# Kernel tuning notes

Hardware: AMD Instinct MI355X
Metric: run time of the kernel (lower is better)

Reference implementation:

```python
import jax, jax.numpy as jnp
import numpy as np


def _cdist_p2(x, y):
    # x: [B, N, D], y: [B, M, D] -> [B, N, M] euclidean distances
    x2 = jnp.sum(x * x, axis=-1, keepdims=True)          # [B, N, 1]
    y2 = jnp.sum(y * y, axis=-1, keepdims=True)          # [B, M, 1]
    xy = jnp.einsum('bnd,bmd->bnm', x, y)                # [B, N, M]
    d2 = x2 + jnp.swapaxes(y2, -1, -2) - 2.0 * xy
    return jnp.sqrt(jnp.maximum(d2, 0.0))


def setup_inputs() -> dict:
    key = jax.random.key(0)
    kx, ky = jax.random.split(key)
    B, N, M, D = 8, 8192, 8192, 64
    x = jax.random.normal(kx, (B, N, D), dtype=jnp.float32)
    y = jax.random.normal(ky, (B, M, D), dtype=jnp.float32)
    return {"x": x, "y": y}


def reference(x, y):
    # relative_distances: [B, N, M]
    rd = _cdist_p2(x, y)
    M = rd.shape[-1]
    a = jnp.min(rd, axis=-1)            # [B, N] nearest y for each x
    b = jnp.min(rd, axis=-2)            # [B, M] nearest x for each y
    loss_per_batch = jnp.sum(a, axis=-1) + jnp.sum(b, axis=-1)  # [B]
    return jnp.mean(loss_per_batch) / M
```

## Files before the change

### kernel.cpp

```cpp
#include <hip/hip_runtime.h>
#include <cstdint>
#include <cstddef>

typedef unsigned short u16;
typedef __attribute__((ext_vector_type(8))) short short8;
typedef __attribute__((ext_vector_type(8))) u16 ushort8;
typedef __attribute__((ext_vector_type(4))) float float4_t;

#define BB 8
#define NN 8192
#define DD 64
#define NTILES 64
#define TILE_SHORTS 8192

__device__ inline u16 f32_to_bf16(float f) {
  unsigned u = __float_as_uint(f);
  u += 0x7FFFu + ((u >> 16) & 1u);
  return (u16)(u >> 16);
}

__device__ inline unsigned enc_ord(float f) {
  unsigned u = __float_as_uint(f);
  return (u & 0x80000000u) ? ~u : (u | 0x80000000u);
}
__device__ inline float dec_ord(unsigned u) {
  return __uint_as_float((u & 0x80000000u) ? (u & 0x7fffffffu) : ~u);
}

__global__ void zero_kernel(unsigned* __restrict__ p, int n) {
  int i = blockIdx.x * 256 + threadIdx.x;
  if (i < n) p[i] = 0u;
}

__global__ __launch_bounds__(256) void pre_kernel(
    const float* __restrict__ x, const float* __restrict__ y,
    u16* __restrict__ xs, u16* __restrict__ ys,
    float* __restrict__ x2h, float* __restrict__ y2h)
{
  const int bid = blockIdx.x;
  const int tid = threadIdx.x;
  const bool isY = bid >= 256;
  const float* src = isY ? y : x;
  u16* dst = isY ? ys : xs;
  float* s2 = isY ? y2h : x2h;

  const int row = ((bid & 255) << 8) | tid;
  const float4* rp = (const float4*)(src + (size_t)row * DD);
  float buf[DD];
  float ss = 0.f;
#pragma unroll
  for (int k = 0; k < 16; ++k) {
    float4 f = rp[k];
    buf[4*k+0] = f.x; buf[4*k+1] = f.y; buf[4*k+2] = f.z; buf[4*k+3] = f.w;
    ss += f.x*f.x + f.y*f.y + f.z*f.z + f.w*f.w;
  }
  s2[row] = 0.5f * ss;

  const int b  = row >> 13;
  const int n  = row & (NN - 1);
  const int nt = n >> 7;
  const int I  = (n >> 4) & 7;
  const int rl = n & 15;
  u16* tb = dst + (size_t)((b << 6) | nt) * TILE_SHORTS;
#pragma unroll
  for (int s = 0; s < 2; ++s)
#pragma unroll
    for (int qq = 0; qq < 4; ++qq) {
      ushort8 o;
#pragma unroll
      for (int j = 0; j < 8; ++j) o[j] = f32_to_bf16(buf[s*32 + qq*8 + j]);
      *(ushort8*)(tb + (I*2 + s)*512 + (qq*16 + rl)*8) = o;
    }
}

__global__ __launch_bounds__(256, 2) void main_kernel(
    const u16* __restrict__ xs, const u16* __restrict__ ys,
    const float* __restrict__ x2h, const float* __restrict__ y2h,
    float* __restrict__ a_min, float* __restrict__ colpart,
    unsigned* __restrict__ colmax_u, const int use_part)
{
  __shared__ __align__(16) u16 ytile[2][TILE_SHORTS];
  __shared__ float colbuf[2][2][128];
  __shared__ float rowbuf[2][128];

  const int bid = blockIdx.x;
  const int b   = bid & 7;
  const int nt  = bid >> 3;
  const int tid = threadIdx.x;
  const int w = tid >> 6, lane = tid & 63;
  const int wr = w >> 1, wc = w & 1;
  const int l15 = lane & 15, q = lane >> 4;
  const int n0 = nt << 7;

  const u16* xs_tile = xs + (size_t)((b << 6) | nt) * TILE_SHORTS;
  short8 afr[4][2];
#pragma unroll
  for (int i = 0; i < 4; ++i)
#pragma unroll
    for (int s = 0; s < 2; ++s)
      afr[i][s] = *(const short8*)(xs_tile + ((wr*4 + i)*2 + s)*512 + lane*8);

  float x2r[4][4];
  const float* x2b = x2h + b*NN + n0 + wr*64;
#pragma unroll
  for (int i = 0; i < 4; ++i)
#pragma unroll
    for (int r = 0; r < 4; ++r) x2r[i][r] = x2b[i*16 + q*4 + r];

  float rowmax[4][4];
#pragma unroll
  for (int i = 0; i < 4; ++i)
#pragma unroll
    for (int r = 0; r < 4; ++r) rowmax[i][r] = -3.0e38f;

  const float* y2b = y2h + b*NN;
  const u16* ys_b  = ys + (size_t)(b << 6) * TILE_SHORTS;

#pragma unroll
  for (int c = 0; c < 4; ++c) {
    const int chunk = w*4 + c;
    __builtin_amdgcn_global_load_lds(
        (const __attribute__((address_space(1))) void*)(ys_b + chunk*512 + lane*8),
        (__attribute__((address_space(3))) void*)(&ytile[0][chunk*512]),
        16, 0, 0);
  }
  __syncthreads();

  const float4_t zero4 = {0.f, 0.f, 0.f, 0.f};
  int cur = 0;
  for (int mt = 0; mt < NTILES; ++mt) {
    if (mt + 1 < NTILES) {
      const u16* g = ys_b + (size_t)(mt + 1) * TILE_SHORTS;
#pragma unroll
      for (int c = 0; c < 4; ++c) {
        const int chunk = w*4 + c;
        __builtin_amdgcn_global_load_lds(
            (const __attribute__((address_space(1))) void*)(g + chunk*512 + lane*8),
            (__attribute__((address_space(3))) void*)(&ytile[cur ^ 1][chunk*512]),
            16, 0, 0);
      }
    }

    float y2c[4];
#pragma unroll
    for (int j = 0; j < 4; ++j) y2c[j] = y2b[(mt << 7) + wc*64 + j*16 + l15];

    short8 bf[4][2];
#pragma unroll
    for (int j = 0; j < 4; ++j)
#pragma unroll
      for (int s = 0; s < 2; ++s)
        bf[j][s] = *(const short8*)(&ytile[cur][((wc*4 + j)*2 + s)*512 + lane*8]);

    float4_t acc[4][4];
#pragma unroll
    for (int i = 0; i < 4; ++i)
#pragma unroll
      for (int j = 0; j < 4; ++j)
        acc[i][j] = __builtin_amdgcn_mfma_f32_16x16x32_bf16(afr[i][0], bf[j][0], zero4, 0, 0, 0);
#pragma unroll
    for (int i = 0; i < 4; ++i)
#pragma unroll
      for (int j = 0; j < 4; ++j)
        acc[i][j] = __builtin_amdgcn_mfma_f32_16x16x32_bf16(afr[i][1], bf[j][1], acc[i][j], 0, 0, 0);

    float cmax[4] = {-3.0e38f, -3.0e38f, -3.0e38f, -3.0e38f};
#pragma unroll
    for (int i = 0; i < 4; ++i)
#pragma unroll
      for (int j = 0; j < 4; ++j)
#pragma unroll
        for (int r = 0; r < 4; ++r) {
          float v = acc[i][j][r];
          rowmax[i][r] = fmaxf(rowmax[i][r], v - y2c[j]);
          cmax[j]      = fmaxf(cmax[j],      v - x2r[i][r]);
        }
#pragma unroll
    for (int j = 0; j < 4; ++j) {
      cmax[j] = fmaxf(cmax[j], __shfl_xor(cmax[j], 16));
      cmax[j] = fmaxf(cmax[j], __shfl_xor(cmax[j], 32));
    }
    float lo = (q & 1) ? cmax[1] : cmax[0];
    float hi = (q & 1) ? cmax[3] : cmax[2];
    float cv = (q & 2) ? hi : lo;
    colbuf[mt & 1][wr][wc*64 + lane] = cv;
    __syncthreads();
    if (tid < 128) {
      float v = fmaxf(colbuf[mt & 1][0][tid], colbuf[mt & 1][1][tid]);
      const int m = (mt << 7) + tid;
      if (use_part) colpart[(size_t)((b << 6) | nt) * NN + m] = v;
      else          atomicMax(&colmax_u[b*NN + m], enc_ord(v));
    }
    cur ^= 1;
  }

#pragma unroll
  for (int i = 0; i < 4; ++i)
#pragma unroll
    for (int r = 0; r < 4; ++r) {
      float v = rowmax[i][r];
      v = fmaxf(v, __shfl_xor(v, 1));
      v = fmaxf(v, __shfl_xor(v, 2));
      v = fmaxf(v, __shfl_xor(v, 4));
      v = fmaxf(v, __shfl_xor(v, 8));
      rowmax[i][r] = v;
    }
  if (l15 == 0) {
#pragma unroll
    for (int i = 0; i < 4; ++i)
#pragma unroll
      for (int r = 0; r < 4; ++r)
        rowbuf[wc][wr*64 + i*16 + q*4 + r] = rowmax[i][r];
  }
  __syncthreads();
  if (tid < 128) {
    float v  = fmaxf(rowbuf[0][tid], rowbuf[1][tid]);
    float x2 = x2h[b*NN + n0 + tid];
    a_min[b*NN + n0 + tid] = sqrtf(fmaxf(2.f*(x2 - v), 0.f));
  }
}

__global__ __launch_bounds__(256) void reduce_kernel(
    const float* __restrict__ colpart, const unsigned* __restrict__ colmax_u,
    const float* __restrict__ y2h, const float* __restrict__ a_min,
    float* __restrict__ partials, const int use_part)
{
  const int bid = blockIdx.x;
  const int tid = threadIdx.x;
  const int b = bid >> 5, mc = bid & 31;
  const int m = (mc << 8) + tid;

  float v;
  if (use_part) {
    v = -3.0e38f;
#pragma unroll 4
    for (int nt = 0; nt < 64; ++nt)
      v = fmaxf(v, colpart[(size_t)((b << 6) | nt) * NN + m]);
  } else {
    v = dec_ord(colmax_u[b*NN + m]);
  }
  float s = sqrtf(fmaxf(2.f*(y2h[b*NN + m] - v), 0.f));
  s += a_min[bid*256 + tid];

#pragma unroll
  for (int d = 1; d < 64; d <<= 1) s += __shfl_xor(s, d);
  __shared__ float wsum[4];
  if ((tid & 63) == 0) wsum[tid >> 6] = s;
  __syncthreads();
  if (tid == 0) partials[bid] = wsum[0] + wsum[1] + wsum[2] + wsum[3];
}

__global__ void final_kernel(const float* __restrict__ partials, float* __restrict__ out) {
  const int tid = threadIdx.x;
  float s = partials[tid];
#pragma unroll
  for (int d = 1; d < 64; d <<= 1) s += __shfl_xor(s, d);
  __shared__ float wsum[4];
  if ((tid & 63) == 0) wsum[tid >> 6] = s;
  __syncthreads();
  if (tid == 0) out[0] = (wsum[0] + wsum[1] + wsum[2] + wsum[3]) * (1.0f / 65536.0f);
}

extern "C" void kernel_launch(void* const* d_in, const int* in_sizes, int n_in,
                              void* d_out, int out_size, void* d_ws, size_t ws_size,
                              hipStream_t stream) {
  const float* x = (const float*)d_in[0];
  const float* y = (const float*)d_in[1];
  float* out = (float*)d_out;

  char* p = (char*)d_ws;
  u16* xs = (u16*)p;            p += (size_t)512 * 16384;
  u16* ys = (u16*)p;            p += (size_t)512 * 16384;
  float* x2h = (float*)p;       p += (size_t)65536 * 4;
  float* y2h = (float*)p;       p += (size_t)65536 * 4;
  float* a_min = (float*)p;     p += (size_t)65536 * 4;
  float* partials = (float*)p;  p += 4096;
  unsigned* colmax_u = (unsigned*)p;
  float* colpart = (float*)p;
  const size_t base = (size_t)(p - (char*)d_ws);
  const int use_part = (ws_size >= base + (size_t)16777216) ? 1 : 0;

  if (!use_part)
    zero_kernel<<<dim3(256), dim3(256), 0, stream>>>(colmax_u, 65536);

  pre_kernel<<<dim3(512), dim3(256), 0, stream>>>(x, y, xs, ys, x2h, y2h);
  main_kernel<<<dim3(512), dim3(256), 0, stream>>>(xs, ys, x2h, y2h, a_min,
                                                   colpart, colmax_u, use_part);
  reduce_kernel<<<dim3(256), dim3(256), 0, stream>>>(colpart, colmax_u, y2h,
                                                     a_min, partials, use_part);
  final_kernel<<<dim3(1), dim3(256), 0, stream>>>(partials, out);
}
```

Baseline: 193.7 us.

## Split main kernel over three M ranges and fold x2 bias into MFMA

The main kernel's M loop is split into three ranges, which triples the grid to 1536 blocks and raises occupancy to 3 blocks per CU. Row-min partials are combined later in the reduce kernel, through partial buffers or atomics. The -x2 term is fed as the MFMA accumulator init, so the column max needs no per-element subtraction. The y2 values are now staged into LDS together with the tile. pre_kernel is also spread over four threads per row to raise parallelism. In exchange the kernel writes more partial data, and the extra occupancy may bring register pressure.

```diff
diff --git a/kernel.cpp b/kernel.cpp
--- a/kernel.cpp
+++ b/kernel.cpp
@@ -12,6 +12,7 @@
 #define DD 64
 #define NTILES 64
 #define TILE_SHORTS 8192
+#define TILE_EXT 8448
 
 __device__ inline u16 f32_to_bf16(float f) {
   unsigned u = __float_as_uint(f);
@@ -39,53 +40,62 @@
 {
   const int bid = blockIdx.x;
   const int tid = threadIdx.x;
-  const bool isY = bid >= 256;
+  const bool isY = bid >= 1024;
   const float* src = isY ? y : x;
   u16* dst = isY ? ys : xs;
   float* s2 = isY ? y2h : x2h;
 
-  const int row = ((bid & 255) << 8) | tid;
-  const float4* rp = (const float4*)(src + (size_t)row * DD);
-  float buf[DD];
+  const int row = ((bid & 1023) << 6) | (tid >> 2);
+  const int kq  = tid & 3;
+
+  const float4* rp = (const float4*)(src + (size_t)row * DD + kq * 16);
+  float buf[16];
   float ss = 0.f;
 #pragma unroll
-  for (int k = 0; k < 16; ++k) {
+  for (int k = 0; k < 4; ++k) {
     float4 f = rp[k];
     buf[4*k+0] = f.x; buf[4*k+1] = f.y; buf[4*k+2] = f.z; buf[4*k+3] = f.w;
     ss += f.x*f.x + f.y*f.y + f.z*f.z + f.w*f.w;
   }
-  s2[row] = 0.5f * ss;
+  ss += __shfl_xor(ss, 1);
+  ss += __shfl_xor(ss, 2);
+  if (kq == 0) s2[row] = 0.5f * ss;
 
   const int b  = row >> 13;
   const int n  = row & (NN - 1);
   const int nt = n >> 7;
   const int I  = (n >> 4) & 7;
   const int rl = n & 15;
+  const int s  = kq >> 1;
+  const int qq0 = (kq & 1) * 2;
   u16* tb = dst + (size_t)((b << 6) | nt) * TILE_SHORTS;
 #pragma unroll
-  for (int s = 0; s < 2; ++s)
-#pragma unroll
-    for (int qq = 0; qq < 4; ++qq) {
-      ushort8 o;
-#pragma unroll
-      for (int j = 0; j < 8; ++j) o[j] = f32_to_bf16(buf[s*32 + qq*8 + j]);
-      *(ushort8*)(tb + (I*2 + s)*512 + (qq*16 + rl)*8) = o;
-    }
-}
-
-__global__ __launch_bounds__(256, 2) void main_kernel(
+  for (int t = 0; t < 2; ++t) {
+    ushort8 o;
+#pragma unroll
+    for (int j = 0; j < 8; ++j) o[j] = f32_to_bf16(buf[t*8 + j]);
+    *(ushort8*)(tb + (I*2 + s)*512 + ((qq0 + t)*16 + rl)*8) = o;
+  }
+}
+
+__global__ __launch_bounds__(256, 3) void main_kernel(
     const u16* __restrict__ xs, const u16* __restrict__ ys,
     const float* __restrict__ x2h, const float* __restrict__ y2h,
-    float* __restrict__ a_min, float* __restrict__ colpart,
-    unsigned* __restrict__ colmax_u, const int use_part)
+    float* __restrict__ rowpart, float* __restrict__ colpart,
+    unsigned* __restrict__ rowmax_u, unsigned* __restrict__ colmax_u,
+    const int use_part)
 {
-  __shared__ __align__(16) u16 ytile[2][TILE_SHORTS];
+  __shared__ __align__(16) u16 ytile[2][TILE_EXT];
   __shared__ float colbuf[2][2][128];
   __shared__ float rowbuf[2][128];
 
   const int bid = blockIdx.x;
   const int b   = bid & 7;
-  const int nt  = bid >> 3;
+  const int nt  = (bid >> 3) & 63;
+  const int h   = bid >> 9;
+  const int mt_start = (h == 0) ? 0 : (h == 1 ? 22 : 43);
+  const int mt_end   = (h == 0) ? 22 : (h == 1 ? 43 : 64);
+
   const int tid = threadIdx.x;
   const int w = tid >> 6, lane = tid & 63;
   const int wr = w >> 1, wc = w & 1;
@@ -100,12 +110,13 @@
     for (int s = 0; s < 2; ++s)
       afr[i][s] = *(const short8*)(xs_tile + ((wr*4 + i)*2 + s)*512 + lane*8);
 
-  float x2r[4][4];
+  float4_t negx2[4];
   const float* x2b = x2h + b*NN + n0 + wr*64;
 #pragma unroll
-  for (int i = 0; i < 4; ++i)
-#pragma unroll
-    for (int r = 0; r < 4; ++r) x2r[i][r] = x2b[i*16 + q*4 + r];
+  for (int i = 0; i < 4; ++i) {
+    float4_t v = *(const float4_t*)(x2b + i*16 + q*4);
+    negx2[i] = {-v[0], -v[1], -v[2], -v[3]};
+  }
 
   float rowmax[4][4];
 #pragma unroll
@@ -116,20 +127,27 @@
   const float* y2b = y2h + b*NN;
   const u16* ys_b  = ys + (size_t)(b << 6) * TILE_SHORTS;
 
-#pragma unroll
-  for (int c = 0; c < 4; ++c) {
-    const int chunk = w*4 + c;
-    __builtin_amdgcn_global_load_lds(
-        (const __attribute__((address_space(1))) void*)(ys_b + chunk*512 + lane*8),
-        (__attribute__((address_space(3))) void*)(&ytile[0][chunk*512]),
-        16, 0, 0);
+  {
+    const u16* g = ys_b + (size_t)mt_start * TILE_SHORTS;
+#pragma unroll
+    for (int c = 0; c < 4; ++c) {
+      const int chunk = w*4 + c;
+      __builtin_amdgcn_global_load_lds(
+          (const __attribute__((address_space(1))) void*)(g + chunk*512 + lane*8),
+          (__attribute__((address_space(3))) void*)(&ytile[0][chunk*512]),
+          16, 0, 0);
+    }
+    if (w == 0 && lane < 32)
+      __builtin_amdgcn_global_load_lds(
+          (const __attribute__((address_space(1))) void*)(y2b + mt_start*128 + lane*4),
+          (__attribute__((address_space(3))) void*)(&ytile[0][TILE_SHORTS]),
+          16, 0, 0);
   }
   __syncthreads();
 
-  const float4_t zero4 = {0.f, 0.f, 0.f, 0.f};
   int cur = 0;
-  for (int mt = 0; mt < NTILES; ++mt) {
-    if (mt + 1 < NTILES) {
+  for (int mt = mt_start; mt < mt_end; ++mt) {
+    if (mt + 1 < mt_end) {
       const u16* g = ys_b + (size_t)(mt + 1) * TILE_SHORTS;
 #pragma unroll
       for (int c = 0; c < 4; ++c) {
@@ -139,11 +157,17 @@
             (__attribute__((address_space(3))) void*)(&ytile[cur ^ 1][chunk*512]),
             16, 0, 0);
       }
-    }
-
+      if (w == 0 && lane < 32)
+        __builtin_amdgcn_global_load_lds(
+            (const __attribute__((address_space(1))) void*)(y2b + (mt+1)*128 + lane*4),
+            (__attribute__((address_space(3))) void*)(&ytile[cur ^ 1][TILE_SHORTS]),
+            16, 0, 0);
+    }
+
+    const float* y2t = (const float*)&ytile[cur][TILE_SHORTS];
     float y2c[4];
 #pragma unroll
-    for (int j = 0; j < 4; ++j) y2c[j] = y2b[(mt << 7) + wc*64 + j*16 + l15];
+    for (int j = 0; j < 4; ++j) y2c[j] = y2t[wc*64 + j*16 + l15];
 
     short8 bf[4][2];
 #pragma unroll
@@ -157,24 +181,33 @@
     for (int i = 0; i < 4; ++i)
 #pragma unroll
       for (int j = 0; j < 4; ++j)
-        acc[i][j] = __builtin_amdgcn_mfma_f32_16x16x32_bf16(afr[i][0], bf[j][0], zero4, 0, 0, 0);
+        acc[i][j] = __builtin_amdgcn_mfma_f32_16x16x32_bf16(afr[i][0], bf[j][0], negx2[i], 0, 0, 0);
 #pragma unroll
     for (int i = 0; i < 4; ++i)
 #pragma unroll
       for (int j = 0; j < 4; ++j)
         acc[i][j] = __builtin_amdgcn_mfma_f32_16x16x32_bf16(afr[i][1], bf[j][1], acc[i][j], 0, 0, 0);
 
-    float cmax[4] = {-3.0e38f, -3.0e38f, -3.0e38f, -3.0e38f};
+    float cmax[4];
+#pragma unroll
+    for (int j = 0; j < 4; ++j) {
+      float m0 = fmaxf(fmaxf(acc[0][j][0], acc[0][j][1]), fmaxf(acc[0][j][2], acc[0][j][3]));
+      float m1 = fmaxf(fmaxf(acc[1][j][0], acc[1][j][1]), fmaxf(acc[1][j][2], acc[1][j][3]));
+      float m2 = fmaxf(fmaxf(acc[2][j][0], acc[2][j][1]), fmaxf(acc[2][j][2], acc[2][j][3]));
+      float m3 = fmaxf(fmaxf(acc[3][j][0], acc[3][j][1]), fmaxf(acc[3][j][2], acc[3][j][3]));
+      cmax[j] = fmaxf(fmaxf(m0, m1), fmaxf(m2, m3));
+    }
 #pragma unroll
     for (int i = 0; i < 4; ++i)
 #pragma unroll
-      for (int j = 0; j < 4; ++j)
-#pragma unroll
-        for (int r = 0; r < 4; ++r) {
-          float v = acc[i][j][r];
-          rowmax[i][r] = fmaxf(rowmax[i][r], v - y2c[j]);
-          cmax[j]      = fmaxf(cmax[j],      v - x2r[i][r]);
-        }
+      for (int r = 0; r < 4; ++r) {
+        float t0 = acc[i][0][r] - y2c[0];
+        float t1 = acc[i][1][r] - y2c[1];
+        float t2 = acc[i][2][r] - y2c[2];
+        float t3 = acc[i][3][r] - y2c[3];
+        rowmax[i][r] = fmaxf(fmaxf(rowmax[i][r], fmaxf(t0, t1)), fmaxf(t2, t3));
+      }
+
 #pragma unroll
     for (int j = 0; j < 4; ++j) {
       cmax[j] = fmaxf(cmax[j], __shfl_xor(cmax[j], 16));
@@ -214,33 +247,40 @@
   }
   __syncthreads();
   if (tid < 128) {
-    float v  = fmaxf(rowbuf[0][tid], rowbuf[1][tid]);
-    float x2 = x2h[b*NN + n0 + tid];
-    a_min[b*NN + n0 + tid] = sqrtf(fmaxf(2.f*(x2 - v), 0.f));
+    float v = fmaxf(rowbuf[0][tid], rowbuf[1][tid]);
+    if (use_part) rowpart[(size_t)(h*512 + (b << 6) + nt) * 128 + tid] = v;
+    else          atomicMax(&rowmax_u[b*NN + n0 + tid], enc_ord(v));
   }
 }
 
 __global__ __launch_bounds__(256) void reduce_kernel(
-    const float* __restrict__ colpart, const unsigned* __restrict__ colmax_u,
-    const float* __restrict__ y2h, const float* __restrict__ a_min,
+    const float* __restrict__ rowpart, const float* __restrict__ colpart,
+    const unsigned* __restrict__ rowmax_u, const unsigned* __restrict__ colmax_u,
+    const float* __restrict__ y2h,
     float* __restrict__ partials, const int use_part)
 {
   const int bid = blockIdx.x;
   const int tid = threadIdx.x;
-  const int b = bid >> 5, mc = bid & 31;
-  const int m = (mc << 8) + tid;
-
-  float v;
+  const int g = bid*256 + tid;
+  const int b = g >> 13, m = g & (NN - 1);
+
+  float vc, vr;
   if (use_part) {
-    v = -3.0e38f;
-#pragma unroll 4
+    vc = -3.0e38f;
+#pragma unroll 8
     for (int nt = 0; nt < 64; ++nt)
-      v = fmaxf(v, colpart[(size_t)((b << 6) | nt) * NN + m]);
+      vc = fmaxf(vc, colpart[(size_t)((b << 6) | nt) * NN + m]);
+    const int nt = m >> 7, r = m & 127;
+    float r0 = rowpart[(size_t)(0*512 + (b << 6) + nt) * 128 + r];
+    float r1 = rowpart[(size_t)(1*512 + (b << 6) + nt) * 128 + r];
+    float r2 = rowpart[(size_t)(2*512 + (b << 6) + nt) * 128 + r];
+    vr = fmaxf(fmaxf(r0, r1), r2);
   } else {
-    v = dec_ord(colmax_u[b*NN + m]);
-  }
-  float s = sqrtf(fmaxf(2.f*(y2h[b*NN + m] - v), 0.f));
-  s += a_min[bid*256 + tid];
+    vc = dec_ord(colmax_u[g]);
+    vr = dec_ord(rowmax_u[g]);
+  }
+  float s = sqrtf(fmaxf(2.f*(y2h[g] - vc), 0.f))
+          + sqrtf(fmaxf(-2.f*vr, 0.f));
 
 #pragma unroll
   for (int d = 1; d < 64; d <<= 1) s += __shfl_xor(s, d);
@@ -273,20 +313,25 @@
   u16* ys = (u16*)p;            p += (size_t)512 * 16384;
   float* x2h = (float*)p;       p += (size_t)65536 * 4;
   float* y2h = (float*)p;       p += (size_t)65536 * 4;
-  float* a_min = (float*)p;     p += (size_t)65536 * 4;
   float* partials = (float*)p;  p += 4096;
-  unsigned* colmax_u = (unsigned*)p;
-  float* colpart = (float*)p;
-  const size_t base = (size_t)(p - (char*)d_ws);
-  const int use_part = (ws_size >= base + (size_t)16777216) ? 1 : 0;
+  char* tail = p;
+  float* rowpart = (float*)tail;
+  float* colpart = (float*)(tail + (size_t)1536 * 128 * 4);
+  unsigned* rowmax_u = (unsigned*)tail;
+  unsigned* colmax_u = (unsigned*)(tail + (size_t)65536 * 4);
+  const size_t need_part = (size_t)(tail - (char*)d_ws) +
+                           (size_t)1536 * 128 * 4 + (size_t)512 * 8192 * 4;
+  const int use_part = (ws_size >= need_part) ? 1 : 0;
 
   if (!use_part)
-    zero_kernel<<<dim3(256), dim3(256), 0, stream>>>(colmax_u, 65536);
-
-  pre_kernel<<<dim3(512), dim3(256), 0, stream>>>(x, y, xs, ys, x2h, y2h);
-  main_kernel<<<dim3(512), dim3(256), 0, stream>>>(xs, ys, x2h, y2h, a_min,
-                                                   colpart, colmax_u, use_part);
-  reduce_kernel<<<dim3(256), dim3(256), 0, stream>>>(colpart, colmax_u, y2h,
-                                                     a_min, partials, use_part);
+    zero_kernel<<<dim3(512), dim3(256), 0, stream>>>(rowmax_u, 131072);
+
+  pre_kernel<<<dim3(2048), dim3(256), 0, stream>>>(x, y, xs, ys, x2h, y2h);
+  main_kernel<<<dim3(1536), dim3(256), 0, stream>>>(xs, ys, x2h, y2h,
+                                                    rowpart, colpart,
+                                                    rowmax_u, colmax_u, use_part);
+  reduce_kernel<<<dim3(256), dim3(256), 0, stream>>>(rowpart, colpart,
+                                                     rowmax_u, colmax_u, y2h,
+                                                     partials, use_part);
   final_kernel<<<dim3(1), dim3(256), 0, stream>>>(partials, out);
 }
```

After: 178.4 us. 1.09x faster.

## Drop LDS staging and per-tile barriers; waves own column slices with register prefetch

Applied to the files above, without the earlier changes.

The main kernel no longer stages y tiles through shared memory with double buffering and a barrier every tile. Each wave now keeps all 128 x rows in registers and reads its own 32-column slice of y straight from global memory, with a one-tile register prefetch. The -x2 term is folded into the MFMA accumulator init, so the column max is taken directly from the accumulators and written without a cross-wave shared-memory reduction or barrier. The pre-kernel is split across four threads per row, and the colmax zeroing is folded into it, which removes a launch. The trade-off is higher register pressure from holding 8 A fragments and larger accumulators, plus repeated global/L2 reads of y with no LDS sharing between waves.

```diff
diff --git a/kernel.cpp b/kernel.cpp
--- a/kernel.cpp
+++ b/kernel.cpp
@@ -27,50 +27,53 @@
   return __uint_as_float((u & 0x80000000u) ? (u & 0x7fffffffu) : ~u);
 }
 
-__global__ void zero_kernel(unsigned* __restrict__ p, int n) {
-  int i = blockIdx.x * 256 + threadIdx.x;
-  if (i < n) p[i] = 0u;
-}
-
 __global__ __launch_bounds__(256) void pre_kernel(
     const float* __restrict__ x, const float* __restrict__ y,
     u16* __restrict__ xs, u16* __restrict__ ys,
-    float* __restrict__ x2h, float* __restrict__ y2h)
+    float* __restrict__ x2h, float* __restrict__ y2h,
+    unsigned* __restrict__ colmax_u, const int use_part)
 {
   const int bid = blockIdx.x;
   const int tid = threadIdx.x;
-  const bool isY = bid >= 256;
+
+  if (!use_part && bid < 256) colmax_u[(bid << 8) | tid] = 0u;
+
+  const bool isY = bid >= 1024;
   const float* src = isY ? y : x;
   u16* dst = isY ? ys : xs;
   float* s2 = isY ? y2h : x2h;
 
-  const int row = ((bid & 255) << 8) | tid;
-  const float4* rp = (const float4*)(src + (size_t)row * DD);
-  float buf[DD];
+  const int row = ((bid & 1023) << 6) | (tid >> 2);
+  const int kq  = tid & 3;
+
+  const float4* rp = (const float4*)(src + (size_t)row * DD + kq * 16);
+  float buf[16];
   float ss = 0.f;
 #pragma unroll
-  for (int k = 0; k < 16; ++k) {
+  for (int k = 0; k < 4; ++k) {
     float4 f = rp[k];
     buf[4*k+0] = f.x; buf[4*k+1] = f.y; buf[4*k+2] = f.z; buf[4*k+3] = f.w;
     ss += f.x*f.x + f.y*f.y + f.z*f.z + f.w*f.w;
   }
-  s2[row] = 0.5f * ss;
+  ss += __shfl_xor(ss, 1);
+  ss += __shfl_xor(ss, 2);
+  if (kq == 0) s2[row] = 0.5f * ss;
 
   const int b  = row >> 13;
   const int n  = row & (NN - 1);
   const int nt = n >> 7;
   const int I  = (n >> 4) & 7;
   const int rl = n & 15;
+  const int s  = kq >> 1;
+  const int qq0 = (kq & 1) * 2;
   u16* tb = dst + (size_t)((b << 6) | nt) * TILE_SHORTS;
 #pragma unroll
-  for (int s = 0; s < 2; ++s)
-#pragma unroll
-    for (int qq = 0; qq < 4; ++qq) {
-      ushort8 o;
-#pragma unroll
-      for (int j = 0; j < 8; ++j) o[j] = f32_to_bf16(buf[s*32 + qq*8 + j]);
-      *(ushort8*)(tb + (I*2 + s)*512 + (qq*16 + rl)*8) = o;
-    }
+  for (int t = 0; t < 2; ++t) {
+    ushort8 o;
+#pragma unroll
+    for (int j = 0; j < 8; ++j) o[j] = f32_to_bf16(buf[t*8 + j]);
+    *(ushort8*)(tb + (I*2 + s)*512 + ((qq0 + t)*16 + rl)*8) = o;
+  }
 }
 
 __global__ __launch_bounds__(256, 2) void main_kernel(
@@ -79,123 +82,115 @@
     float* __restrict__ a_min, float* __restrict__ colpart,
     unsigned* __restrict__ colmax_u, const int use_part)
 {
-  __shared__ __align__(16) u16 ytile[2][TILE_SHORTS];
-  __shared__ float colbuf[2][2][128];
-  __shared__ float rowbuf[2][128];
+  __shared__ float rowbuf[4][128];
 
   const int bid = blockIdx.x;
   const int b   = bid & 7;
   const int nt  = bid >> 3;
   const int tid = threadIdx.x;
   const int w = tid >> 6, lane = tid & 63;
-  const int wr = w >> 1, wc = w & 1;
   const int l15 = lane & 15, q = lane >> 4;
   const int n0 = nt << 7;
 
   const u16* xs_tile = xs + (size_t)((b << 6) | nt) * TILE_SHORTS;
-  short8 afr[4][2];
-#pragma unroll
-  for (int i = 0; i < 4; ++i)
+  short8 afr[8][2];
+#pragma unroll
+  for (int i = 0; i < 8; ++i)
 #pragma unroll
     for (int s = 0; s < 2; ++s)
-      afr[i][s] = *(const short8*)(xs_tile + ((wr*4 + i)*2 + s)*512 + lane*8);
-
-  float x2r[4][4];
-  const float* x2b = x2h + b*NN + n0 + wr*64;
-#pragma unroll
-  for (int i = 0; i < 4; ++i)
-#pragma unroll
-    for (int r = 0; r < 4; ++r) x2r[i][r] = x2b[i*16 + q*4 + r];
-
-  float rowmax[4][4];
-#pragma unroll
-  for (int i = 0; i < 4; ++i)
+      afr[i][s] = *(const short8*)(xs_tile + (i*2 + s)*512 + lane*8);
+
+  float4_t negx2[8];
+  const float* x2b = x2h + b*NN + n0;
+#pragma unroll
+  for (int i = 0; i < 8; ++i) {
+    float4_t v = *(const float4_t*)(x2b + i*16 + q*4);
+    negx2[i] = {-v[0], -v[1], -v[2], -v[3]};
+  }
+
+  float rowmax[8][4];
+#pragma unroll
+  for (int i = 0; i < 8; ++i)
 #pragma unroll
     for (int r = 0; r < 4; ++r) rowmax[i][r] = -3.0e38f;
 
   const float* y2b = y2h + b*NN;
   const u16* ys_b  = ys + (size_t)(b << 6) * TILE_SHORTS;
-
-#pragma unroll
-  for (int c = 0; c < 4; ++c) {
-    const int chunk = w*4 + c;
-    __builtin_amdgcn_global_load_lds(
-        (const __attribute__((address_space(1))) void*)(ys_b + chunk*512 + lane*8),
-        (__attribute__((address_space(3))) void*)(&ytile[0][chunk*512]),
-        16, 0, 0);
-  }
-  __syncthreads();
-
-  const float4_t zero4 = {0.f, 0.f, 0.f, 0.f};
-  int cur = 0;
+  float* colp      = colpart + (size_t)((b << 6) | nt) * NN;
+  unsigned* colu   = colmax_u + b*NN;
+
+  short8 bcur[2][2];
+  float y2cur[2];
+#pragma unroll
+  for (int j = 0; j < 2; ++j) {
+#pragma unroll
+    for (int s = 0; s < 2; ++s)
+      bcur[j][s] = *(const short8*)(ys_b + ((2*w + j)*2 + s)*512 + lane*8);
+    y2cur[j] = y2b[w*32 + j*16 + l15];
+  }
+
   for (int mt = 0; mt < NTILES; ++mt) {
-    if (mt + 1 < NTILES) {
-      const u16* g = ys_b + (size_t)(mt + 1) * TILE_SHORTS;
-#pragma unroll
-      for (int c = 0; c < 4; ++c) {
-        const int chunk = w*4 + c;
-        __builtin_amdgcn_global_load_lds(
-            (const __attribute__((address_space(1))) void*)(g + chunk*512 + lane*8),
-            (__attribute__((address_space(3))) void*)(&ytile[cur ^ 1][chunk*512]),
-            16, 0, 0);
+    const int mtn = (mt + 1 < NTILES) ? (mt + 1) : 0;
+    short8 bnext[2][2];
+    float y2next[2];
+    const u16* g = ys_b + (size_t)mtn * TILE_SHORTS;
+#pragma unroll
+    for (int j = 0; j < 2; ++j) {
+#pragma unroll
+      for (int s = 0; s < 2; ++s)
+        bnext[j][s] = *(const short8*)(g + ((2*w + j)*2 + s)*512 + lane*8);
+      y2next[j] = y2b[mtn*128 + w*32 + j*16 + l15];
+    }
+
+    float cmax[2];
+#pragma unroll
+    for (int j = 0; j < 2; ++j) {
+      float4_t acc[8];
+#pragma unroll
+      for (int i = 0; i < 8; ++i)
+        acc[i] = __builtin_amdgcn_mfma_f32_16x16x32_bf16(afr[i][0], bcur[j][0], negx2[i], 0, 0, 0);
+#pragma unroll
+      for (int i = 0; i < 8; ++i)
+        acc[i] = __builtin_amdgcn_mfma_f32_16x16x32_bf16(afr[i][1], bcur[j][1], acc[i], 0, 0, 0);
+
+      float m01 = fmaxf(fmaxf(acc[0][0], acc[0][1]), fmaxf(acc[0][2], acc[0][3]));
+#pragma unroll
+      for (int i = 1; i < 8; ++i) {
+        float mi = fmaxf(fmaxf(acc[i][0], acc[i][1]), fmaxf(acc[i][2], acc[i][3]));
+        m01 = fmaxf(m01, mi);
       }
-    }
-
-    float y2c[4];
-#pragma unroll
-    for (int j = 0; j < 4; ++j) y2c[j] = y2b[(mt << 7) + wc*64 + j*16 + l15];
-
-    short8 bf[4][2];
-#pragma unroll
-    for (int j = 0; j < 4; ++j)
-#pragma unroll
-      for (int s = 0; s < 2; ++s)
-        bf[j][s] = *(const short8*)(&ytile[cur][((wc*4 + j)*2 + s)*512 + lane*8]);
-
-    float4_t acc[4][4];
-#pragma unroll
-    for (int i = 0; i < 4; ++i)
-#pragma unroll
-      for (int j = 0; j < 4; ++j)
-        acc[i][j] = __builtin_amdgcn_mfma_f32_16x16x32_bf16(afr[i][0], bf[j][0], zero4, 0, 0, 0);
-#pragma unroll
-    for (int i = 0; i < 4; ++i)
-#pragma unroll
-      for (int j = 0; j < 4; ++j)
-        acc[i][j] = __builtin_amdgcn_mfma_f32_16x16x32_bf16(afr[i][1], bf[j][1], acc[i][j], 0, 0, 0);
-
-    float cmax[4] = {-3.0e38f, -3.0e38f, -3.0e38f, -3.0e38f};
-#pragma unroll
-    for (int i = 0; i < 4; ++i)
-#pragma unroll
-      for (int j = 0; j < 4; ++j)
-#pragma unroll
-        for (int r = 0; r < 4; ++r) {
-          float v = acc[i][j][r];
-          rowmax[i][r] = fmaxf(rowmax[i][r], v - y2c[j]);
-          cmax[j]      = fmaxf(cmax[j],      v - x2r[i][r]);
-        }
-#pragma unroll
-    for (int j = 0; j < 4; ++j) {
+      cmax[j] = m01;
+
+      const float y2j = y2cur[j];
+#pragma unroll
+      for (int i = 0; i < 8; ++i)
+#pragma unroll
+        for (int r = 0; r < 4; ++r)
+          rowmax[i][r] = fmaxf(rowmax[i][r], acc[i][r] - y2j);
+    }
+
+#pragma unroll
+    for (int j = 0; j < 2; ++j) {
       cmax[j] = fmaxf(cmax[j], __shfl_xor(cmax[j], 16));
       cmax[j] = fmaxf(cmax[j], __shfl_xor(cmax[j], 32));
     }
-    float lo = (q & 1) ? cmax[1] : cmax[0];
-    float hi = (q & 1) ? cmax[3] : cmax[2];
-    float cv = (q & 2) ? hi : lo;
-    colbuf[mt & 1][wr][wc*64 + lane] = cv;
-    __syncthreads();
-    if (tid < 128) {
-      float v = fmaxf(colbuf[mt & 1][0][tid], colbuf[mt & 1][1][tid]);
-      const int m = (mt << 7) + tid;
-      if (use_part) colpart[(size_t)((b << 6) | nt) * NN + m] = v;
-      else          atomicMax(&colmax_u[b*NN + m], enc_ord(v));
-    }
-    cur ^= 1;
-  }
-
-#pragma unroll
-  for (int i = 0; i < 4; ++i)
+    float cv = (q & 1) ? cmax[1] : cmax[0];
+    const int m = (mt << 7) + w*32 + q*16 + l15;
+    if (q < 2) {
+      if (use_part) colp[m] = cv;
+      else          atomicMax(&colu[m], enc_ord(cv));
+    }
+
+#pragma unroll
+    for (int j = 0; j < 2; ++j) {
+#pragma unroll
+      for (int s = 0; s < 2; ++s) bcur[j][s] = bnext[j][s];
+      y2cur[j] = y2next[j];
+    }
+  }
+
+#pragma unroll
+  for (int i = 0; i < 8; ++i)
 #pragma unroll
     for (int r = 0; r < 4; ++r) {
       float v = rowmax[i][r];
@@ -207,16 +202,16 @@
     }
   if (l15 == 0) {
 #pragma unroll
-    for (int i = 0; i < 4; ++i)
+    for (int i = 0; i < 8; ++i)
 #pragma unroll
       for (int r = 0; r < 4; ++r)
-        rowbuf[wc][wr*64 + i*16 + q*4 + r] = rowmax[i][r];
+        rowbuf[w][i*16 + q*4 + r] = rowmax[i][r];
   }
   __syncthreads();
   if (tid < 128) {
-    float v  = fmaxf(rowbuf[0][tid], rowbuf[1][tid]);
-    float x2 = x2h[b*NN + n0 + tid];
-    a_min[b*NN + n0 + tid] = sqrtf(fmaxf(2.f*(x2 - v), 0.f));
+    float v = fmaxf(fmaxf(rowbuf[0][tid], rowbuf[1][tid]),
+                    fmaxf(rowbuf[2][tid], rowbuf[3][tid]));
+    a_min[b*NN + n0 + tid] = sqrtf(fmaxf(-2.f * v, 0.f));
   }
 }
 
@@ -227,20 +222,20 @@
 {
   const int bid = blockIdx.x;
   const int tid = threadIdx.x;
-  const int b = bid >> 5, mc = bid & 31;
-  const int m = (mc << 8) + tid;
-
-  float v;
+  const int g = bid*256 + tid;
+  const int b = g >> 13, m = g & (NN - 1);
+
+  float vc;
   if (use_part) {
-    v = -3.0e38f;
-#pragma unroll 4
+    vc = -3.0e38f;
+#pragma unroll 8
     for (int nt = 0; nt < 64; ++nt)
-      v = fmaxf(v, colpart[(size_t)((b << 6) | nt) * NN + m]);
+      vc = fmaxf(vc, colpart[(size_t)((b << 6) | nt) * NN + m]);
   } else {
-    v = dec_ord(colmax_u[b*NN + m]);
-  }
-  float s = sqrtf(fmaxf(2.f*(y2h[b*NN + m] - v), 0.f));
-  s += a_min[bid*256 + tid];
+    vc = dec_ord(colmax_u[g]);
+  }
+  float s = sqrtf(fmaxf(2.f*(y2h[g] - vc), 0.f))
+          + a_min[g];
 
 #pragma unroll
   for (int d = 1; d < 64; d <<= 1) s += __shfl_xor(s, d);
@@ -275,15 +270,14 @@
   float* y2h = (float*)p;       p += (size_t)65536 * 4;
   float* a_min = (float*)p;     p += (size_t)65536 * 4;
   float* partials = (float*)p;  p += 4096;
-  unsigned* colmax_u = (unsigned*)p;
-  float* colpart = (float*)p;
-  const size_t base = (size_t)(p - (char*)d_ws);
-  const int use_part = (ws_size >= base + (size_t)16777216) ? 1 : 0;
-
-  if (!use_part)
-    zero_kernel<<<dim3(256), dim3(256), 0, stream>>>(colmax_u, 65536);
-
-  pre_kernel<<<dim3(512), dim3(256), 0, stream>>>(x, y, xs, ys, x2h, y2h);
+  char* tail = p;
+  float* colpart = (float*)tail;
+  unsigned* colmax_u = (unsigned*)tail;
+  const size_t need_part = (size_t)(tail - (char*)d_ws) + (size_t)512 * 8192 * 4;
+  const int use_part = (ws_size >= need_part) ? 1 : 0;
+
+  pre_kernel<<<dim3(2048), dim3(256), 0, stream>>>(x, y, xs, ys, x2h, y2h,
+                                                   colmax_u, use_part);
   main_kernel<<<dim3(512), dim3(256), 0, stream>>>(xs, ys, x2h, y2h, a_min,
                                                    colpart, colmax_u, use_part);
   reduce_kernel<<<dim3(256), dim3(256), 0, stream>>>(colpart, colmax_u, y2h,
```

Result: faster. 168.8 us (-12.9%).
